# Kernel tuning notes

Hardware: AMD Instinct MI355X
Metric: run time of the kernel (lower is better)

## Reference

```python
import jax, jax.numpy as jnp
import numpy as np

D_MODEL = 1024
D_HIDDEN = 4096
N_EXPERTS = 8
B, S = 2, 2048


def setup_inputs() -> dict:
    key = jax.random.key(0)
    ks = jax.random.split(key, 4)
    sd = 1.0 / np.sqrt(D_MODEL)
    sh = 1.0 / np.sqrt(D_HIDDEN)
    return {
        "x": jax.random.normal(ks[0], (B, S, D_MODEL), dtype=jnp.float32),
        "Wg": jax.random.normal(ks[1], (D_MODEL, N_EXPERTS), dtype=jnp.float32) * sd,
        "bg": jnp.zeros((N_EXPERTS,), dtype=jnp.float32),
        "W1": jax.random.normal(ks[2], (N_EXPERTS, D_MODEL, D_HIDDEN), dtype=jnp.float32) * sd,
        "b1": jnp.zeros((N_EXPERTS, D_HIDDEN), dtype=jnp.float32),
        "W2": jax.random.normal(ks[3], (N_EXPERTS, D_HIDDEN, D_MODEL), dtype=jnp.float32) * sh,
        "b2": jnp.zeros((N_EXPERTS, D_MODEL), dtype=jnp.float32),
    }


def reference(x, Wg, bg, W1, b1, W2, b2):
    # Router: softmax is monotone, so argmax(softmax(logits)) == argmax(logits).
    logits = jnp.einsum("bsd,de->bse", x, Wg) + bg
    expert_idx = jnp.argmax(logits, axis=-1)  # [B, S]
    # Top-1 dispatch, expressed as compute-all-experts + per-token select
    # (jit-friendly; the torch loop masks/gathers per expert).
    h = jax.nn.gelu(jnp.einsum("bsd,edh->bseh", x, W1) + b1, approximate=False)
    y = jnp.einsum("bseh,ehd->bsed", h, W2) + b2  # [B, S, E, D]
    out = jnp.take_along_axis(y, expert_idx[:, :, None, None], axis=2)[:, :, 0, :]
    return out
```

## Files before the change

### kernel.cpp

```cpp
#include <hip/hip_runtime.h>
#include <hip/hip_bf16.h>
#include <math.h>

#define D_MODEL 1024
#define D_HIDDEN 4096
#define N_EXP 8
#define N_TOK 4096
#define MBS 40

typedef __attribute__((ext_vector_type(8))) __bf16 bf16x8_t;
typedef __attribute__((ext_vector_type(4))) float f32x4_t;

#define WS_PREFIX_OFF 128
#define WS_BUCKET_OFF 256
#define WS_XB_OFF     ((size_t)1 << 18)
#define WS_HT_OFF     (((size_t)1 << 18) + ((size_t)8 << 20))
#define WS_W1T_OFF    (((size_t)1 << 18) + ((size_t)50 << 20))
#define WS_W2T_OFF    (((size_t)1 << 18) + ((size_t)114 << 20))
#define WS_AE_OFF     (((size_t)1 << 18) + ((size_t)178 << 20))
#define WS_NEED       (((size_t)1 << 18) + ((size_t)189 << 20))

__device__ __forceinline__ void gload16(const void* g, void* l) {
    __builtin_amdgcn_global_load_lds(
        (__attribute__((address_space(1))) void*)(g),
        (__attribute__((address_space(3))) void*)(l),
        16, 0, 0);
}

__global__ __launch_bounds__(64) void init_counts(int* counts) {
    if (threadIdx.x < N_EXP) counts[threadIdx.x] = 0;
}

__global__ __launch_bounds__(64) void prefix_kernel(const int* counts, int* prefix) {
    if (threadIdx.x == 0) {
        int s = 0;
        prefix[0] = 0;
#pragma unroll
        for (int e = 0; e < N_EXP; ++e) { s += (counts[e] + 127) >> 7; prefix[e + 1] = s; }
    }
}

__global__ __launch_bounds__(256) void router_kernel(
    const float* __restrict__ x, const float* __restrict__ Wg,
    const float* __restrict__ bg, int* __restrict__ counts,
    int* __restrict__ bucket, __hip_bfloat16* __restrict__ xb)
{
    const int wid  = threadIdx.x >> 6;
    const int lane = threadIdx.x & 63;
    const int t    = blockIdx.x * 4 + wid;
    const float* xr = x + (size_t)t * D_MODEL;

    double acc[N_EXP];
#pragma unroll
    for (int e = 0; e < N_EXP; ++e) acc[e] = 0.0;

#pragma unroll
    for (int j = 0; j < D_MODEL / 64; ++j) {
        const int d = j * 64 + lane;
        const float xv = xr[d];
        xb[(size_t)t * D_MODEL + d] = __float2bfloat16(xv);
        const float4* wr = (const float4*)(Wg + (size_t)d * N_EXP);
        const float4 w0 = wr[0], w1 = wr[1];
        const double xd = (double)xv;
        acc[0] += xd * (double)w0.x; acc[1] += xd * (double)w0.y;
        acc[2] += xd * (double)w0.z; acc[3] += xd * (double)w0.w;
        acc[4] += xd * (double)w1.x; acc[5] += xd * (double)w1.y;
        acc[6] += xd * (double)w1.z; acc[7] += xd * (double)w1.w;
    }
#pragma unroll
    for (int e = 0; e < N_EXP; ++e) {
        double v = acc[e];
#pragma unroll
        for (int off = 32; off >= 1; off >>= 1) v += __shfl_xor(v, off, 64);
        acc[e] = v + (double)bg[e];
    }
    if (lane == 0) {
        int best = 0; double bv = acc[0];
#pragma unroll
        for (int e = 1; e < N_EXP; ++e)
            if (acc[e] > bv) { bv = acc[e]; best = e; }
        const int pos = atomicAdd(&counts[best], 1);
        bucket[best * N_TOK + pos] = t;
    }
}

template<int KT, int NT>
__global__ __launch_bounds__(256) void convert_w(
    const float* __restrict__ W, __hip_bfloat16* __restrict__ Wt)
{
    constexpr int NB = NT / 128, KC = KT / 64;
    const int nblk = blockIdx.x, kc = blockIdx.y, e = blockIdx.z;
    const int k0 = kc * 64, n0 = nblk * 128;
    const int tid = threadIdx.x;
    __shared__ __hip_bfloat16 Lt[128 * 68];

    const int nq  = tid & 31;
    const int kq2 = tid >> 5;
#pragma unroll
    for (int h = 0; h < 2; ++h) {
        const int kq = kq2 + h * 8;
        const float* src = W + (size_t)e * KT * NT + (size_t)(k0 + kq * 4) * NT + n0 + nq * 4;
        const float4 v0 = *(const float4*)(src);
        const float4 v1 = *(const float4*)(src + (size_t)NT);
        const float4 v2 = *(const float4*)(src + (size_t)2 * NT);
        const float4 v3 = *(const float4*)(src + (size_t)3 * NT);
#pragma unroll
        for (int i = 0; i < 4; ++i) {
            const int n = nq * 4 + i;
            union { __hip_bfloat16 hh[4]; unsigned long long u; } pk;
            pk.hh[0] = __float2bfloat16(((const float*)&v0)[i]);
            pk.hh[1] = __float2bfloat16(((const float*)&v1)[i]);
            pk.hh[2] = __float2bfloat16(((const float*)&v2)[i]);
            pk.hh[3] = __float2bfloat16(((const float*)&v3)[i]);
            *(unsigned long long*)((char*)Lt + (size_t)n * 136 + kq * 8) = pk.u;
        }
    }
    __syncthreads();

    char* outc = (char*)Wt + (((size_t)e * NB + nblk) * KC + kc) * 16384;
    const int n = tid >> 1, half = tid & 1;
#pragma unroll
    for (int s = 0; s < 4; ++s) {
        const int slot = half * 4 + s;
        const int ko = slot ^ (n & 7);
        const uint4 v = *(const uint4*)((const char*)Lt + (size_t)n * 136 + ko * 16);
        *(uint4*)(outc + (size_t)n * 128 + slot * 16) = v;
    }
}

__global__ __launch_bounds__(256) void gather_a(
    const float* __restrict__ x, const int* __restrict__ counts,
    const int* __restrict__ prefix, const int* __restrict__ bucket,
    __hip_bfloat16* __restrict__ Ae)
{
    const int mbg = blockIdx.x, kc = blockIdx.y;
    if (mbg >= prefix[8]) return;
    int e = 0;
#pragma unroll
    for (int q = 1; q < 8; ++q) if (mbg >= prefix[q]) e = q;
    const int cnt  = counts[e];
    const int mblk = mbg - prefix[e];
    const int tid  = threadIdx.x;
    const int m = tid >> 1, half = tid & 1;
    int idx = mblk * 128 + m;
    if (idx >= cnt) idx = cnt - 1;
    const int tok = bucket[e * N_TOK + idx];
    const float* src = x + (size_t)tok * D_MODEL + kc * 64 + half * 32;
    char* dst = (char*)Ae + ((size_t)mbg * 16 + kc) * 16384 + (size_t)m * 128;
#pragma unroll
    for (int s = 0; s < 4; ++s) {
        const float4 a = *(const float4*)(src + s * 8);
        const float4 b = *(const float4*)(src + s * 8 + 4);
        union { __hip_bfloat16 hh[8]; uint4 u; } pk;
#pragma unroll
        for (int j = 0; j < 4; ++j) {
            pk.hh[j]     = __float2bfloat16(((const float*)&a)[j]);
            pk.hh[j + 4] = __float2bfloat16(((const float*)&b)[j]);
        }
        const int ko = half * 4 + s;
        *(uint4*)(dst + ((ko ^ (m & 7)) << 4)) = pk.u;
    }
}

template<int K_TOT, int N_TOT, int SPLITS, bool IS_FFN1>
__global__ __launch_bounds__(256, 2) void ffn_gemm_w(
    const __hip_bfloat16* __restrict__ At,
    const __hip_bfloat16* __restrict__ Wt,
    const float* __restrict__ bias,
    const int* __restrict__ counts,
    const int* __restrict__ prefix,
    __hip_bfloat16* __restrict__ hout,
    float* __restrict__ pout)
{
    constexpr int KC     = K_TOT / 64;
    constexpr int KSTEPS = KC / SPLITS;
    constexpr int NBW    = N_TOT / 256;
    constexpr int NB128  = N_TOT / 128;
    constexpr int NWG    = NBW * SPLITS * MBS;

    const int orig = blockIdx.x;
    const int wg   = (orig & 7) * (NWG >> 3) + (orig >> 3);
    const int nblk = wg / (SPLITS * MBS);
    const int r2   = wg % (SPLITS * MBS);
    const int split = r2 / MBS;
    const int mbg   = r2 % MBS;
    if (mbg >= prefix[8]) return;
    int e = 0;
#pragma unroll
    for (int q = 1; q < 8; ++q) if (mbg >= prefix[q]) e = q;
    const int n0 = nblk * 256;

    const int tid  = threadIdx.x;
    const int lane = tid & 63;
    const int wid  = tid >> 6;
    const int wm   = wid >> 1, wn = wid & 1;

    __shared__ char As[16384];
    __shared__ char Bs[32768];

    const char* Ab  = (const char*)At + ((size_t)mbg * KC + split * KSTEPS) * 16384;
    const char* Bb0 = (const char*)Wt + (((size_t)e * NB128 + nblk * 2) * KC + split * KSTEPS) * 16384;
    const char* Bb1 = Bb0 + (size_t)KC * 16384;
    const int off = wid * 4096 + lane * 16;
    char* lA  = As + wid * 4096;
    char* lB0 = Bs + wid * 4096;
    char* lB1 = Bs + 16384 + wid * 4096;

    f32x4_t acc[4][8];
#pragma unroll
    for (int f = 0; f < 4; ++f)
#pragma unroll
        for (int g = 0; g < 8; ++g) acc[f][g] = (f32x4_t){0.f, 0.f, 0.f, 0.f};

    for (int t = 0; t < KSTEPS; ++t) {
        const char* Ac = Ab  + (size_t)t * 16384 + off;
        const char* B0 = Bb0 + (size_t)t * 16384 + off;
        const char* B1 = Bb1 + (size_t)t * 16384 + off;
#pragma unroll
        for (int i = 0; i < 4; ++i) gload16(Ac + i * 1024, lA + i * 1024);
#pragma unroll
        for (int i = 0; i < 4; ++i) gload16(B0 + i * 1024, lB0 + i * 1024);
#pragma unroll
        for (int i = 0; i < 4; ++i) gload16(B1 + i * 1024, lB1 + i * 1024);
        __syncthreads();

#pragma unroll
        for (int kk = 0; kk < 2; ++kk) {
            uint4 af[4], bf[8];
            const int ko = kk * 4 + (lane >> 4);
#pragma unroll
            for (int f = 0; f < 4; ++f) {
                const int r = wm * 64 + f * 16 + (lane & 15);
                af[f] = *(const uint4*)(As + r * 128 + ((ko ^ (r & 7)) << 4));
            }
#pragma unroll
            for (int g = 0; g < 8; ++g) {
                const int n = wn * 128 + g * 16 + (lane & 15);
                bf[g] = *(const uint4*)(Bs + n * 128 + ((ko ^ (n & 7)) << 4));
            }
#pragma unroll
            for (int f = 0; f < 4; ++f)
#pragma unroll
                for (int g = 0; g < 8; ++g)
                    acc[f][g] = __builtin_amdgcn_mfma_f32_16x16x32_bf16(
                        __builtin_bit_cast(bf16x8_t, af[f]),
                        __builtin_bit_cast(bf16x8_t, bf[g]),
                        acc[f][g], 0, 0, 0);
        }
        __syncthreads();
    }

    if (IS_FFN1) {
        char* hb = (char*)hout + (size_t)mbg * (D_HIDDEN / 64) * 16384;
#pragma unroll
        for (int f = 0; f < 4; ++f) {
#pragma unroll
            for (int j = 0; j < 4; ++j) {
                const int m = wm * 64 + f * 16 + (lane >> 4) * 4 + j;
#pragma unroll
                for (int g = 0; g < 8; ++g) {
                    const int col = n0 + wn * 128 + g * 16 + (lane & 15);
                    float v = acc[f][g][j] + bias[e * N_TOT + col];
                    v = 0.5f * v * (1.0f + erff(v * 0.70710678118654752f));
                    const int kc = col >> 6, kw = col & 63, ko = kw >> 3, b = kw & 7;
                    *(__hip_bfloat16*)(hb + ((size_t)kc * 128 + m) * 128 +
                                       (((ko ^ (m & 7)) << 4) + (b << 1))) = __float2bfloat16(v);
                }
            }
        }
    } else {
        float* pb = pout + ((size_t)(split * MBS + mbg) * 128) * 1024;
#pragma unroll
        for (int f = 0; f < 4; ++f) {
#pragma unroll
            for (int j = 0; j < 4; ++j) {
                const int m = wm * 64 + f * 16 + (lane >> 4) * 4 + j;
#pragma unroll
                for (int g = 0; g < 8; ++g) {
                    const int col = n0 + wn * 128 + g * 16 + (lane & 15);
                    pb[(size_t)m * 1024 + col] = acc[f][g][j];
                }
            }
        }
    }
}

__global__ __launch_bounds__(256) void reduce_out(
    const float* __restrict__ P, const float* __restrict__ b2,
    const int* __restrict__ counts, const int* __restrict__ prefix,
    const int* __restrict__ bucket, float* __restrict__ out)
{
    const int slot = blockIdx.x;
    if (slot >= prefix[8]) return;
    int e = 0;
#pragma unroll
    for (int q = 1; q < 8; ++q) if (slot >= prefix[q]) e = q;
    const int cnt  = counts[e];
    const int mblk = slot - prefix[e];
    const int r    = blockIdx.y * 4 + (threadIdx.x >> 6);
    const int idx  = mblk * 128 + r;
    if (idx >= cnt) return;
    const int tok  = bucket[e * N_TOK + idx];
    const int lane = threadIdx.x & 63;
    const float* p0 = P + ((size_t)slot * 128 + r) * 1024;
    const float* p1 = P + ((size_t)(MBS + slot) * 128 + r) * 1024;
    const float* bb = b2 + e * 1024;
    float* op = out + (size_t)tok * 1024;
#pragma unroll
    for (int j = 0; j < 4; ++j) {
        const int c = j * 256 + lane * 4;
        const float4 a = *(const float4*)(p0 + c);
        const float4 b = *(const float4*)(p1 + c);
        const float4 w = *(const float4*)(bb + c);
        float4 v;
        v.x = a.x + b.x + w.x; v.y = a.y + b.y + w.y;
        v.z = a.z + b.z + w.z; v.w = a.w + b.w + w.w;
        *(float4*)(op + c) = v;
    }
}

template<int K_TOT, int N_TOT, bool IS_FFN1>
__global__ __launch_bounds__(256, 2) void ffn_gemm_f32(
    const __hip_bfloat16* __restrict__ A,
    const float* __restrict__ W,
    const float* __restrict__ bias,
    const int* __restrict__ counts,
    const int* __restrict__ bucket,
    __hip_bfloat16* __restrict__ hout,
    float* __restrict__ yout)
{
    const int e   = blockIdx.z;
    const int cnt = counts[e];
    const int m0  = blockIdx.y * 128;
    if (m0 >= cnt) return;
    const int n0   = blockIdx.x * 128;
    const int tid  = threadIdx.x;
    const int lane = tid & 63;
    const int wid  = tid >> 6;
    const int wm   = wid >> 1, wn = wid & 1;

    __shared__ __hip_bfloat16 As[128 * 64];
    __shared__ __hip_bfloat16 Bs[128 * 64];
    __shared__ int s_tok[128];

    if (tid < 128) {
        int idx = m0 + tid;
        if (idx >= cnt) idx = cnt - 1;
        s_tok[tid] = bucket[e * N_TOK + idx];
    }
    __syncthreads();

    const __hip_bfloat16* gA[4]; char* lA[4];
#pragma unroll
    for (int i = 0; i < 4; ++i) {
        const int r = wid * 32 + i * 8 + (lane >> 3);
        gA[i] = A + (size_t)s_tok[r] * K_TOT + (((lane & 7) ^ (r & 7)) << 3);
        lA[i] = (char*)As + (size_t)(wid * 32 + i * 8) * 128;
    }
    const int ko_t = lane & 7;
    const int nq   = wid * 8 + (lane >> 3);
    const float* wb = W + (size_t)e * K_TOT * N_TOT + (size_t)(ko_t * 8) * N_TOT + n0 + nq * 4;

    f32x4_t acc[4][4];
#pragma unroll
    for (int f = 0; f < 4; ++f)
#pragma unroll
        for (int g = 0; g < 4; ++g) acc[f][g] = (f32x4_t){0.f, 0.f, 0.f, 0.f};

    for (int k0 = 0; k0 < K_TOT; k0 += 64) {
#pragma unroll
        for (int i = 0; i < 4; ++i) gload16(gA[i] + k0, lA[i]);
        const float* wk = wb + (size_t)k0 * N_TOT;
        float4 v[8];
#pragma unroll
        for (int j = 0; j < 8; ++j) v[j] = *(const float4*)(wk + (size_t)j * N_TOT);
#pragma unroll
        for (int i = 0; i < 4; ++i) {
            const int n = nq * 4 + i;
            union { __hip_bfloat16 hh[8]; uint4 u; } pk;
#pragma unroll
            for (int j = 0; j < 8; ++j) pk.hh[j] = __float2bfloat16(((const float*)&v[j])[i]);
            *(uint4*)((char*)Bs + n * 128 + ((ko_t ^ (n & 7)) << 4)) = pk.u;
        }
        __syncthreads();

#pragma unroll
        for (int kk = 0; kk < 2; ++kk) {
            uint4 af[4], bf[4];
            const int ko = kk * 4 + (lane >> 4);
#pragma unroll
            for (int f = 0; f < 4; ++f) {
                const int r = wm * 64 + f * 16 + (lane & 15);
                af[f] = *(const uint4*)((const char*)As + r * 128 + ((ko ^ (r & 7)) << 4));
            }
#pragma unroll
            for (int g = 0; g < 4; ++g) {
                const int n = wn * 64 + g * 16 + (lane & 15);
                bf[g] = *(const uint4*)((const char*)Bs + n * 128 + ((ko ^ (n & 7)) << 4));
            }
#pragma unroll
            for (int f = 0; f < 4; ++f)
#pragma unroll
                for (int g = 0; g < 4; ++g)
                    acc[f][g] = __builtin_amdgcn_mfma_f32_16x16x32_bf16(
                        __builtin_bit_cast(bf16x8_t, af[f]),
                        __builtin_bit_cast(bf16x8_t, bf[g]),
                        acc[f][g], 0, 0, 0);
        }
        __syncthreads();
    }

#pragma unroll
    for (int f = 0; f < 4; ++f) {
#pragma unroll
        for (int j = 0; j < 4; ++j) {
            const int rl = wm * 64 + f * 16 + (lane >> 4) * 4 + j;
            const bool ok = (m0 + rl) < cnt;
            const int tok = s_tok[rl];
#pragma unroll
            for (int g = 0; g < 4; ++g) {
                const int col = n0 + wn * 64 + g * 16 + (lane & 15);
                float v = acc[f][g][j] + bias[e * N_TOT + col];
                if (IS_FFN1) {
                    v = 0.5f * v * (1.0f + erff(v * 0.70710678118654752f));
                    if (ok) hout[(size_t)tok * N_TOT + col] = __float2bfloat16(v);
                } else {
                    if (ok) yout[(size_t)tok * N_TOT + col] = v;
                }
            }
        }
    }
}

extern "C" void kernel_launch(void* const* d_in, const int* in_sizes, int n_in,
                              void* d_out, int out_size, void* d_ws, size_t ws_size,
                              hipStream_t stream) {
    const float* x  = (const float*)d_in[0];
    const float* Wg = (const float*)d_in[1];
    const float* bg = (const float*)d_in[2];
    const float* W1 = (const float*)d_in[3];
    const float* b1 = (const float*)d_in[4];
    const float* W2 = (const float*)d_in[5];
    const float* b2 = (const float*)d_in[6];
    float* out = (float*)d_out;

    char* ws = (char*)d_ws;
    int* counts = (int*)(ws);
    int* prefix = (int*)(ws + WS_PREFIX_OFF);
    int* bucket = (int*)(ws + WS_BUCKET_OFF);
    __hip_bfloat16* xb  = (__hip_bfloat16*)(ws + WS_XB_OFF);
    __hip_bfloat16* ht  = (__hip_bfloat16*)(ws + WS_HT_OFF);
    __hip_bfloat16* w1t = (__hip_bfloat16*)(ws + WS_W1T_OFF);
    __hip_bfloat16* w2t = (__hip_bfloat16*)(ws + WS_W2T_OFF);
    __hip_bfloat16* ae  = (__hip_bfloat16*)(ws + WS_AE_OFF);
    float* partials     = (float*)(ws + WS_W1T_OFF);

    init_counts<<<dim3(1), dim3(64), 0, stream>>>(counts);
    router_kernel<<<dim3(N_TOK / 4), dim3(256), 0, stream>>>(x, Wg, bg, counts, bucket, xb);
    prefix_kernel<<<dim3(1), dim3(64), 0, stream>>>(counts, prefix);

    if (ws_size >= WS_NEED) {
        convert_w<D_MODEL, D_HIDDEN><<<dim3(32, 16, N_EXP), dim3(256), 0, stream>>>(W1, w1t);
        convert_w<D_HIDDEN, D_MODEL><<<dim3(8, 64, N_EXP), dim3(256), 0, stream>>>(W2, w2t);
        gather_a<<<dim3(MBS, 16), dim3(256), 0, stream>>>(x, counts, prefix, bucket, ae);
        ffn_gemm_w<D_MODEL, D_HIDDEN, 1, true>
            <<<dim3(MBS * (D_HIDDEN / 256)), dim3(256), 0, stream>>>(
                ae, w1t, b1, counts, prefix, ht, nullptr);
        ffn_gemm_w<D_HIDDEN, D_MODEL, 2, false>
            <<<dim3(MBS * (D_MODEL / 256) * 2), dim3(256), 0, stream>>>(
                ht, w2t, nullptr, counts, prefix, nullptr, partials);
        reduce_out<<<dim3(MBS, 32), dim3(256), 0, stream>>>(
            partials, b2, counts, prefix, bucket, out);
    } else {
        __hip_bfloat16* h = ht;
        ffn_gemm_f32<D_MODEL, D_HIDDEN, true>
            <<<dim3(D_HIDDEN / 128, N_TOK / 128, N_EXP), dim3(256), 0, stream>>>(
                xb, W1, b1, counts, bucket, h, nullptr);
        ffn_gemm_f32<D_HIDDEN, D_MODEL, false>
            <<<dim3(D_MODEL / 128, N_TOK / 128, N_EXP), dim3(256), 0, stream>>>(
                h, W2, b2, counts, bucket, nullptr, out);
    }
}
```

Before: 333.8 us.

## Enlarge expert GEMM M-tile to 256 rows using 512-thread workgroups

Token bucket blocks grow from 128 to 256 rows. The prefix, gather, weight-conversion layout, GEMM and reduce kernels are all reindexed to match. The GEMM now runs 8 waves per workgroup, and each workgroup loads a full 256-column B tile per k-step. This doubles B-tile reuse per loaded weight byte and cuts the number of workgroups, but adds more padding waste per expert. It also raises register and LDS pressure under the 512-thread launch bounds. Workspace offsets are reshuffled so ht aliases the xb region, and the fallback path gets its own buffer.

```diff
diff --git a/kernel.cpp b/kernel.cpp
--- a/kernel.cpp
+++ b/kernel.cpp
@@ -6,19 +6,20 @@
 #define D_HIDDEN 4096
 #define N_EXP 8
 #define N_TOK 4096
-#define MBS 40
+#define MBS2 24
 
 typedef __attribute__((ext_vector_type(8))) __bf16 bf16x8_t;
 typedef __attribute__((ext_vector_type(4))) float f32x4_t;
 
 #define WS_PREFIX_OFF 128
 #define WS_BUCKET_OFF 256
+#define WS_HT_OFF     ((size_t)1 << 18)
 #define WS_XB_OFF     ((size_t)1 << 18)
-#define WS_HT_OFF     (((size_t)1 << 18) + ((size_t)8 << 20))
-#define WS_W1T_OFF    (((size_t)1 << 18) + ((size_t)50 << 20))
-#define WS_W2T_OFF    (((size_t)1 << 18) + ((size_t)114 << 20))
-#define WS_AE_OFF     (((size_t)1 << 18) + ((size_t)178 << 20))
-#define WS_NEED       (((size_t)1 << 18) + ((size_t)189 << 20))
+#define WS_HFB_OFF    (((size_t)1 << 18) + ((size_t)8 << 20))
+#define WS_W1T_OFF    (((size_t)1 << 18) + ((size_t)48 << 20))
+#define WS_W2T_OFF    (((size_t)1 << 18) + ((size_t)112 << 20))
+#define WS_AE_OFF     (((size_t)1 << 18) + ((size_t)176 << 20))
+#define WS_NEED       (((size_t)1 << 18) + ((size_t)188 << 20))
 
 __device__ __forceinline__ void gload16(const void* g, void* l) {
     __builtin_amdgcn_global_load_lds(
@@ -36,7 +37,7 @@
         int s = 0;
         prefix[0] = 0;
 #pragma unroll
-        for (int e = 0; e < N_EXP; ++e) { s += (counts[e] + 127) >> 7; prefix[e + 1] = s; }
+        for (int e = 0; e < N_EXP; ++e) { s += (counts[e] + 255) >> 8; prefix[e + 1] = s; }
     }
 }
 
@@ -88,9 +89,10 @@
 __global__ __launch_bounds__(256) void convert_w(
     const float* __restrict__ W, __hip_bfloat16* __restrict__ Wt)
 {
-    constexpr int NB = NT / 128, KC = KT / 64;
-    const int nblk = blockIdx.x, kc = blockIdx.y, e = blockIdx.z;
-    const int k0 = kc * 64, n0 = nblk * 128;
+    constexpr int NB = NT / 256, KC = KT / 64;
+    const int nb128 = blockIdx.x, kc = blockIdx.y, e = blockIdx.z;
+    const int k0 = kc * 64, n0 = nb128 * 128;
+    const int nb = n0 >> 8, halfc = (n0 >> 7) & 1;
     const int tid = threadIdx.x;
     __shared__ __hip_bfloat16 Lt[128 * 68];
 
@@ -117,7 +119,7 @@
     }
     __syncthreads();
 
-    char* outc = (char*)Wt + (((size_t)e * NB + nblk) * KC + kc) * 16384;
+    char* outc = (char*)Wt + (((size_t)e * NB + nb) * KC + kc) * 32768 + halfc * 16384;
     const int n = tid >> 1, half = tid & 1;
 #pragma unroll
     for (int s = 0; s < 4; ++s) {
@@ -133,7 +135,7 @@
     const int* __restrict__ prefix, const int* __restrict__ bucket,
     __hip_bfloat16* __restrict__ Ae)
 {
-    const int mbg = blockIdx.x, kc = blockIdx.y;
+    const int mbg = blockIdx.x >> 1, halfm = blockIdx.x & 1, kc = blockIdx.y;
     if (mbg >= prefix[8]) return;
     int e = 0;
 #pragma unroll
@@ -141,12 +143,13 @@
     const int cnt  = counts[e];
     const int mblk = mbg - prefix[e];
     const int tid  = threadIdx.x;
-    const int m = tid >> 1, half = tid & 1;
-    int idx = mblk * 128 + m;
+    const int m = halfm * 128 + (tid >> 1);
+    const int half = tid & 1;
+    int idx = mblk * 256 + m;
     if (idx >= cnt) idx = cnt - 1;
     const int tok = bucket[e * N_TOK + idx];
     const float* src = x + (size_t)tok * D_MODEL + kc * 64 + half * 32;
-    char* dst = (char*)Ae + ((size_t)mbg * 16 + kc) * 16384 + (size_t)m * 128;
+    char* dst = (char*)Ae + ((size_t)mbg * 16 + kc) * 32768 + (size_t)m * 128;
 #pragma unroll
     for (int s = 0; s < 4; ++s) {
         const float4 a = *(const float4*)(src + s * 8);
@@ -163,27 +166,25 @@
 }
 
 template<int K_TOT, int N_TOT, int SPLITS, bool IS_FFN1>
-__global__ __launch_bounds__(256, 2) void ffn_gemm_w(
+__global__ __launch_bounds__(512, 2) void ffn_gemm_q(
     const __hip_bfloat16* __restrict__ At,
     const __hip_bfloat16* __restrict__ Wt,
     const float* __restrict__ bias,
-    const int* __restrict__ counts,
     const int* __restrict__ prefix,
     __hip_bfloat16* __restrict__ hout,
     float* __restrict__ pout)
 {
     constexpr int KC     = K_TOT / 64;
     constexpr int KSTEPS = KC / SPLITS;
-    constexpr int NBW    = N_TOT / 256;
-    constexpr int NB128  = N_TOT / 128;
-    constexpr int NWG    = NBW * SPLITS * MBS;
+    constexpr int NB     = N_TOT / 256;
+    constexpr int NWG    = NB * SPLITS * MBS2;
 
     const int orig = blockIdx.x;
     const int wg   = (orig & 7) * (NWG >> 3) + (orig >> 3);
-    const int nblk = wg / (SPLITS * MBS);
-    const int r2   = wg % (SPLITS * MBS);
-    const int split = r2 / MBS;
-    const int mbg   = r2 % MBS;
+    const int nblk = wg / (SPLITS * MBS2);
+    const int r2   = wg % (SPLITS * MBS2);
+    const int split = r2 / MBS2;
+    const int mbg   = r2 % MBS2;
     if (mbg >= prefix[8]) return;
     int e = 0;
 #pragma unroll
@@ -195,16 +196,14 @@
     const int wid  = tid >> 6;
     const int wm   = wid >> 1, wn = wid & 1;
 
-    __shared__ char As[16384];
+    __shared__ char As[32768];
     __shared__ char Bs[32768];
 
-    const char* Ab  = (const char*)At + ((size_t)mbg * KC + split * KSTEPS) * 16384;
-    const char* Bb0 = (const char*)Wt + (((size_t)e * NB128 + nblk * 2) * KC + split * KSTEPS) * 16384;
-    const char* Bb1 = Bb0 + (size_t)KC * 16384;
+    const char* Ab = (const char*)At + ((size_t)mbg * KC + split * KSTEPS) * 32768;
+    const char* Bb = (const char*)Wt + (((size_t)e * NB + nblk) * KC + split * KSTEPS) * 32768;
     const int off = wid * 4096 + lane * 16;
-    char* lA  = As + wid * 4096;
-    char* lB0 = Bs + wid * 4096;
-    char* lB1 = Bs + 16384 + wid * 4096;
+    char* lA = As + wid * 4096;
+    char* lB = Bs + wid * 4096;
 
     f32x4_t acc[4][8];
 #pragma unroll
@@ -213,15 +212,12 @@
         for (int g = 0; g < 8; ++g) acc[f][g] = (f32x4_t){0.f, 0.f, 0.f, 0.f};
 
     for (int t = 0; t < KSTEPS; ++t) {
-        const char* Ac = Ab  + (size_t)t * 16384 + off;
-        const char* B0 = Bb0 + (size_t)t * 16384 + off;
-        const char* B1 = Bb1 + (size_t)t * 16384 + off;
+        const char* Ac = Ab + (size_t)t * 32768 + off;
+        const char* Bc = Bb + (size_t)t * 32768 + off;
 #pragma unroll
         for (int i = 0; i < 4; ++i) gload16(Ac + i * 1024, lA + i * 1024);
 #pragma unroll
-        for (int i = 0; i < 4; ++i) gload16(B0 + i * 1024, lB0 + i * 1024);
-#pragma unroll
-        for (int i = 0; i < 4; ++i) gload16(B1 + i * 1024, lB1 + i * 1024);
+        for (int i = 0; i < 4; ++i) gload16(Bc + i * 1024, lB + i * 1024);
         __syncthreads();
 
 #pragma unroll
@@ -251,7 +247,7 @@
     }
 
     if (IS_FFN1) {
-        char* hb = (char*)hout + (size_t)mbg * (D_HIDDEN / 64) * 16384;
+        char* hb = (char*)hout + (size_t)mbg * (D_HIDDEN / 64) * 32768;
 #pragma unroll
         for (int f = 0; f < 4; ++f) {
 #pragma unroll
@@ -263,13 +259,13 @@
                     float v = acc[f][g][j] + bias[e * N_TOT + col];
                     v = 0.5f * v * (1.0f + erff(v * 0.70710678118654752f));
                     const int kc = col >> 6, kw = col & 63, ko = kw >> 3, b = kw & 7;
-                    *(__hip_bfloat16*)(hb + ((size_t)kc * 128 + m) * 128 +
+                    *(__hip_bfloat16*)(hb + (size_t)kc * 32768 + (size_t)m * 128 +
                                        (((ko ^ (m & 7)) << 4) + (b << 1))) = __float2bfloat16(v);
                 }
             }
         }
     } else {
-        float* pb = pout + ((size_t)(split * MBS + mbg) * 128) * 1024;
+        float* pb = pout + ((size_t)(split * MBS2 + mbg) * 256) * 1024;
 #pragma unroll
         for (int f = 0; f < 4; ++f) {
 #pragma unroll
@@ -298,12 +294,12 @@
     const int cnt  = counts[e];
     const int mblk = slot - prefix[e];
     const int r    = blockIdx.y * 4 + (threadIdx.x >> 6);
-    const int idx  = mblk * 128 + r;
+    const int idx  = mblk * 256 + r;
     if (idx >= cnt) return;
     const int tok  = bucket[e * N_TOK + idx];
     const int lane = threadIdx.x & 63;
-    const float* p0 = P + ((size_t)slot * 128 + r) * 1024;
-    const float* p1 = P + ((size_t)(MBS + slot) * 128 + r) * 1024;
+    const float* p0 = P + ((size_t)slot * 256 + r) * 1024;
+    const float* p1 = P + ((size_t)(MBS2 + slot) * 256 + r) * 1024;
     const float* bb = b2 + e * 1024;
     float* op = out + (size_t)tok * 1024;
 #pragma unroll
@@ -450,6 +446,7 @@
     int* bucket = (int*)(ws + WS_BUCKET_OFF);
     __hip_bfloat16* xb  = (__hip_bfloat16*)(ws + WS_XB_OFF);
     __hip_bfloat16* ht  = (__hip_bfloat16*)(ws + WS_HT_OFF);
+    __hip_bfloat16* hfb = (__hip_bfloat16*)(ws + WS_HFB_OFF);
     __hip_bfloat16* w1t = (__hip_bfloat16*)(ws + WS_W1T_OFF);
     __hip_bfloat16* w2t = (__hip_bfloat16*)(ws + WS_W2T_OFF);
     __hip_bfloat16* ae  = (__hip_bfloat16*)(ws + WS_AE_OFF);
@@ -462,22 +459,21 @@
     if (ws_size >= WS_NEED) {
         convert_w<D_MODEL, D_HIDDEN><<<dim3(32, 16, N_EXP), dim3(256), 0, stream>>>(W1, w1t);
         convert_w<D_HIDDEN, D_MODEL><<<dim3(8, 64, N_EXP), dim3(256), 0, stream>>>(W2, w2t);
-        gather_a<<<dim3(MBS, 16), dim3(256), 0, stream>>>(x, counts, prefix, bucket, ae);
-        ffn_gemm_w<D_MODEL, D_HIDDEN, 1, true>
-            <<<dim3(MBS * (D_HIDDEN / 256)), dim3(256), 0, stream>>>(
-                ae, w1t, b1, counts, prefix, ht, nullptr);
-        ffn_gemm_w<D_HIDDEN, D_MODEL, 2, false>
-            <<<dim3(MBS * (D_MODEL / 256) * 2), dim3(256), 0, stream>>>(
-                ht, w2t, nullptr, counts, prefix, nullptr, partials);
-        reduce_out<<<dim3(MBS, 32), dim3(256), 0, stream>>>(
+        gather_a<<<dim3(MBS2 * 2, 16), dim3(256), 0, stream>>>(x, counts, prefix, bucket, ae);
+        ffn_gemm_q<D_MODEL, D_HIDDEN, 1, true>
+            <<<dim3(MBS2 * (D_HIDDEN / 256)), dim3(512), 0, stream>>>(
+                ae, w1t, b1, prefix, ht, nullptr);
+        ffn_gemm_q<D_HIDDEN, D_MODEL, 2, false>
+            <<<dim3(MBS2 * (D_MODEL / 256) * 2), dim3(512), 0, stream>>>(
+                ht, w2t, nullptr, prefix, nullptr, partials);
+        reduce_out<<<dim3(MBS2, 64), dim3(256), 0, stream>>>(
             partials, b2, counts, prefix, bucket, out);
     } else {
-        __hip_bfloat16* h = ht;
         ffn_gemm_f32<D_MODEL, D_HIDDEN, true>
             <<<dim3(D_HIDDEN / 128, N_TOK / 128, N_EXP), dim3(256), 0, stream>>>(
-                xb, W1, b1, counts, bucket, h, nullptr);
+                xb, W1, b1, counts, bucket, hfb, nullptr);
         ffn_gemm_f32<D_HIDDEN, D_MODEL, false>
             <<<dim3(D_MODEL / 128, N_TOK / 128, N_EXP), dim3(256), 0, stream>>>(
-                h, W2, b2, counts, bucket, nullptr, out);
-    }
-}
+                hfb, W2, b2, counts, bucket, nullptr, out);
+    }
+}
```

Result: slower. 374.2 us (+12.1%).
